# Kernel optimization log

Hardware: AMD Instinct MI355X
Metric: run time of the kernel (lower is better)

The kernel has to match this reference:

```python
import jax, jax.numpy as jnp
import numpy as np

B, CIN, COUT, K, E, H, W = 32, 128, 256, 3, 8, 64, 64


def setup_inputs() -> dict:
    key = jax.random.key(0)
    k1, k2, k3, k4 = jax.random.split(key, 4)
    x = jax.random.normal(k1, (B, CIN, H, W), dtype=jnp.float32)
    expert_weight = jax.random.normal(k2, (E, COUT, CIN, K, K), dtype=jnp.float32)
    # nn.Linear(in_channels, num_experts): weight [E, CIN], bias [E]
    bound = 1.0 / np.sqrt(CIN)
    routing_w = jax.random.uniform(k3, (E, CIN), minval=-bound, maxval=bound, dtype=jnp.float32)
    routing_b = jax.random.uniform(k4, (E,), minval=-bound, maxval=bound, dtype=jnp.float32)
    return {"x": x, "expert_weight": expert_weight, "routing_w": routing_w, "routing_b": routing_b}


def reference(x, expert_weight, routing_w, routing_b):
    # routing: global-avg-pool -> linear -> softmax over experts
    pooled = x.mean(axis=(2, 3))                             # [B, CIN]
    logits = pooled @ routing_w.T + routing_b                # [B, E]
    rweights = jax.nn.softmax(logits, axis=-1)               # [B, E]
    # per-sample combined conv weights: [B, COUT, CIN, K, K]
    cw = jnp.einsum('be,eoikl->boikl', rweights, expert_weight)

    def conv_one(xi, wi):
        # xi: [CIN, H, W], wi: [COUT, CIN, K, K]; VALID conv, stride 1
        return jax.lax.conv_general_dilated(
            xi[None], wi, window_strides=(1, 1), padding='VALID',
            dimension_numbers=('NCHW', 'OIHW', 'NCHW'))[0]

    return jax.vmap(conv_one)(x, cw)                         # [B, COUT, H-K+1, W-K+1]
```

## Files before the change

### kernel.cpp

```cpp
#include <hip/hip_runtime.h>
#include <hip/hip_bf16.h>


#define CC_B    32
#define CC_CIN  128
#define CC_COUT 256
#define CC_NP   3844
#define CC_NT   18

typedef __attribute__((ext_vector_type(8))) short bf16x8;
typedef __attribute__((ext_vector_type(4))) float f32x4;

__global__ void cc_nhwc(const float* __restrict__ x, __hip_bfloat16* __restrict__ xn,
                        float* __restrict__ psum) {
    const int b = blockIdx.x >> 6, y = blockIdx.x & 63;
    __shared__ float lds[64 * 129];
    __shared__ float sred[256];
    const int t = threadIdx.x;
    const float* src = x + (size_t)b * CC_CIN * 4096 + y * 64;
#pragma unroll
    for (int i = 0; i < 32; ++i) {
        const int idx = i * 256 + t;
        const int cin = idx >> 6, xx = idx & 63;
        lds[xx * 129 + cin] = src[(size_t)cin * 4096 + xx];
    }
    __syncthreads();
    __hip_bfloat16* dst = xn + ((size_t)b * 4096 + y * 64) * CC_CIN;
#pragma unroll
    for (int j = 0; j < 4; ++j) {
        const int cidx = j * 256 + t;
        const int xx = cidx >> 4, c8 = (cidx & 15) * 8;
        union { __hip_bfloat16 h[8]; uint4 v; } u;
#pragma unroll
        for (int jj = 0; jj < 8; ++jj) u.h[jj] = __float2bfloat16(lds[xx * 129 + c8 + jj]);
        *reinterpret_cast<uint4*>(dst + (size_t)xx * CC_CIN + c8) = u.v;
    }
    const int cin = t & 127, xh = (t >> 7) * 32;
    float s = 0.f;
#pragma unroll
    for (int xx = 0; xx < 32; ++xx) s += lds[(xh + xx) * 129 + cin];
    sred[t] = s;
    __syncthreads();
    if (t < 128) psum[((size_t)b * 64 + y) * CC_CIN + t] = sred[t] + sred[t + 128];
}

__global__ void cc_route(const float* __restrict__ psum,
                         const float* __restrict__ rw_w,
                         const float* __restrict__ rw_b,
                         float* __restrict__ rweights) {
    const int b = blockIdx.x, c = threadIdx.x;
    __shared__ float pl[128];
    __shared__ float lg[8];
    const float* p = psum + (size_t)b * 64 * CC_CIN + c;
    float s = 0.f;
#pragma unroll 8
    for (int y = 0; y < 64; ++y) s += p[(size_t)y * CC_CIN];
    pl[c] = s * (1.f / 4096.f);
    __syncthreads();
    if (c < 8) {
        const float* w = rw_w + c * CC_CIN;
        float a = rw_b[c];
#pragma unroll 8
        for (int i = 0; i < CC_CIN; ++i) a += pl[i] * w[i];
        lg[c] = a;
    }
    __syncthreads();
    if (c == 0) {
        float m = lg[0];
#pragma unroll
        for (int e = 1; e < 8; ++e) m = fmaxf(m, lg[e]);
        float ex[8], sm = 0.f;
#pragma unroll
        for (int e = 0; e < 8; ++e) { ex[e] = __expf(lg[e] - m); sm += ex[e]; }
#pragma unroll
        for (int e = 0; e < 8; ++e) rweights[b * 8 + e] = ex[e] / sm;
    }
}

__global__ void cc_combine(const float* __restrict__ ew,
                           const float* __restrict__ rw,
                           __hip_bfloat16* __restrict__ cw) {
    const int t9 = blockIdx.x >> 8;
    const int cout = blockIdx.x & 255;
    const int cin = threadIdx.x;
    __shared__ float rws[256];
    rws[cin] = rw[cin];
    rws[cin + 128] = rw[cin + 128];
    __syncthreads();
    float wv[8];
    const size_t base = ((size_t)cout * CC_CIN + cin) * 9 + t9;
#pragma unroll
    for (int e = 0; e < 8; ++e) wv[e] = ew[base + (size_t)e * (CC_COUT * CC_CIN * 9)];
#pragma unroll 4
    for (int b = 0; b < CC_B; ++b) {
        float acc = 0.f;
#pragma unroll
        for (int e = 0; e < 8; ++e) acc += rws[b * 8 + e] * wv[e];
        cw[(((size_t)b * 9 + t9) * CC_COUT + cout) * CC_CIN + cin] = __float2bfloat16(acc);
    }
}

__device__ __forceinline__ void gload_lds16(const void* g, void* l) {
    __builtin_amdgcn_global_load_lds(
        (const __attribute__((address_space(1))) unsigned int*)g,
        (__attribute__((address_space(3))) unsigned int*)l, 16, 0, 0);
}

__global__ __launch_bounds__(256, 2) void cc_conv(
    const __hip_bfloat16* __restrict__ xn,
    const __hip_bfloat16* __restrict__ cw,
    float* __restrict__ out)
{
    __shared__ __align__(16) char smem[73728];
    const int l   = blockIdx.x;
    const int xcd = l & 7, li = l >> 3;
    const int b   = 4 * xcd + li / 50;
    const int r2  = li % 50;
    const int nt  = r2 >> 1, mt = r2 & 1;
    const int m0  = mt * 128;
    const int n0  = nt * 160;

    const int tid = threadIdx.x;
    const int wid = tid >> 6, lane = tid & 63;
    const int waveM = wid >> 1, waveN = wid & 1;

    f32x4 acc[4][5];
#pragma unroll
    for (int i = 0; i < 4; ++i)
#pragma unroll
        for (int j = 0; j < 5; ++j) acc[i][j] = (f32x4){0.f, 0.f, 0.f, 0.f};

    const int gsw = (lane & 7) ^ (lane >> 3);
    int laOff[4], lbOff[5];
#pragma unroll
    for (int i = 0; i < 4; ++i) {
        const int row = wid * 32 + i * 8 + (lane >> 3);
        laOff[i] = (m0 + row) * CC_CIN + gsw * 8;
    }
#pragma unroll
    for (int i = 0; i < 5; ++i) {
        const int row = wid * 40 + i * 8 + (lane >> 3);
        int p = n0 + row; if (p > CC_NP - 1) p = CC_NP - 1;
        const int oy = p / 62, ox = p - oy * 62;
        lbOff[i] = (oy * 64 + ox) * CC_CIN + gsw * 8;
    }

    const __hip_bfloat16* cwb = cw + (size_t)b * 9 * CC_COUT * CC_CIN;
    const __hip_bfloat16* xnb = xn + (size_t)b * 4096 * CC_CIN;

    auto stageK = [&](int t) {
        const int t9 = t >> 1;
        const int ky = (t9 * 11) >> 5;
        const int kx = t9 - ky * 3;
        const int aoff = t9 * (CC_COUT * CC_CIN) + (t & 1) * 64;
        const int boff = (ky * 64 + kx) * CC_CIN + (t & 1) * 64;
        char* Ab = smem + (t & 1) * 16384 + wid * 4096;
        char* Bb = smem + 32768 + (t & 1) * 20480 + wid * 5120;
#pragma unroll
        for (int i = 0; i < 4; ++i)
            gload_lds16(cwb + aoff + laOff[i], Ab + i * 1024);
#pragma unroll
        for (int i = 0; i < 5; ++i)
            gload_lds16(xnb + boff + lbOff[i], Bb + i * 1024);
    };

    const int rl = lane & 15, q = lane >> 4;

    stageK(0);
    stageK(1);

#pragma unroll
    for (int t = 0; t < CC_NT; ++t) {
        const char* Ab = smem + (t & 1) * 16384;
        const char* Bb = smem + 32768 + (t & 1) * 20480;

        if (t < CC_NT - 1) asm volatile("s_waitcnt vmcnt(9)" ::: "memory");
        else               asm volatile("s_waitcnt vmcnt(0)" ::: "memory");
        asm volatile("s_barrier" ::: "memory");

        bf16x8 af[8], bf[10];
#pragma unroll
        for (int mf = 0; mf < 4; ++mf)
#pragma unroll
            for (int kk = 0; kk < 2; ++kk) {
                const int r = waveM * 64 + mf * 16 + rl;
                af[mf * 2 + kk] = *(const bf16x8*)(Ab + r * 128 + (((kk * 4 + q) ^ (r & 7)) * 16));
            }
#pragma unroll
        for (int nf = 0; nf < 5; ++nf)
#pragma unroll
            for (int kk = 0; kk < 2; ++kk) {
                const int r = waveN * 80 + nf * 16 + rl;
                bf[nf * 2 + kk] = *(const bf16x8*)(Bb + r * 128 + (((kk * 4 + q) ^ (r & 7)) * 16));
            }
        __builtin_amdgcn_s_setprio(1);
#pragma unroll
        for (int kk = 0; kk < 2; ++kk)
#pragma unroll
            for (int mf = 0; mf < 4; ++mf)
#pragma unroll
                for (int nf = 0; nf < 5; ++nf)
                    acc[mf][nf] = __builtin_amdgcn_mfma_f32_16x16x32_bf16(
                        af[mf * 2 + kk], bf[nf * 2 + kk], acc[mf][nf], 0, 0, 0);
        __builtin_amdgcn_s_setprio(0);

        asm volatile("s_waitcnt lgkmcnt(0)" ::: "memory");
        asm volatile("s_barrier" ::: "memory");
        if (t + 2 < CC_NT) stageK(t + 2);
    }

    const int q4 = (lane >> 4) * 4;
#pragma unroll
    for (int mf = 0; mf < 4; ++mf) {
        const int crow = m0 + waveM * 64 + mf * 16 + q4;
#pragma unroll
        for (int nf = 0; nf < 5; ++nf) {
            const int p = n0 + waveN * 80 + nf * 16 + (lane & 15);
            if (p < CC_NP) {
                const size_t ob = ((size_t)b * CC_COUT + crow) * CC_NP + p;
#pragma unroll
                for (int j = 0; j < 4; ++j) out[ob + (size_t)j * CC_NP] = acc[mf][nf][j];
            }
        }
    }
}

extern "C" void kernel_launch(void* const* d_in, const int* in_sizes, int n_in,
                              void* d_out, int out_size, void* d_ws, size_t ws_size,
                              hipStream_t stream) {
    const float* x   = (const float*)d_in[0];
    const float* ew  = (const float*)d_in[1];
    const float* rww = (const float*)d_in[2];
    const float* rwb = (const float*)d_in[3];
    float* out = (float*)d_out;
    char* ws = (char*)d_ws;

    __hip_bfloat16* xnhwc = (__hip_bfloat16*)ws;
    __hip_bfloat16* cwcmb = (__hip_bfloat16*)(ws + 33554432);
    float* psum   = (float*)(ws + 52428800);
    float* rwts   = (float*)(ws + 53493760);

    cc_nhwc<<<dim3(CC_B * 64), dim3(256), 0, stream>>>(x, xnhwc, psum);
    cc_route<<<dim3(CC_B), dim3(128), 0, stream>>>(psum, rww, rwb, rwts);
    cc_combine<<<dim3(9 * CC_COUT), dim3(128), 0, stream>>>(ew, rwts, cwcmb);
    cc_conv<<<dim3(1600), dim3(256), 0, stream>>>(xnhwc, cwcmb, out);
}
```

Before: 124.4 us.

## Load conv input fragments directly to registers, keep only weights in LDS

The B operand (input pixels) is no longer staged through LDS. Each lane now loads its bf16x8 fragments straight from global memory into a double-buffered register array, one step ahead of use. The weight tile still goes through LDS, but the pipeline is restructured so the next A stage is issued right after the barrier, and LDS shrinks from 72KB to 32KB. This removes LDS write/read traffic and one barrier per step, and may allow more resident blocks. The cost is many more VGPRs for the double-buffered B fragments, uncoalesced 16-byte global loads with overlap across kernel taps, and vmcnt counts that must match the exact order in which loads are issued.

```diff
diff --git a/kernel.cpp b/kernel.cpp
--- a/kernel.cpp
+++ b/kernel.cpp
@@ -111,7 +111,7 @@
     const __hip_bfloat16* __restrict__ cw,
     float* __restrict__ out)
 {
-    __shared__ __align__(16) char smem[73728];
+    __shared__ __align__(16) char smem[32768];
     const int l   = blockIdx.x;
     const int xcd = l & 7, li = l >> 3;
     const int b   = 4 * xcd + li / 50;
@@ -131,54 +131,63 @@
         for (int j = 0; j < 5; ++j) acc[i][j] = (f32x4){0.f, 0.f, 0.f, 0.f};
 
     const int gsw = (lane & 7) ^ (lane >> 3);
-    int laOff[4], lbOff[5];
+    int laOff[4];
 #pragma unroll
     for (int i = 0; i < 4; ++i) {
         const int row = wid * 32 + i * 8 + (lane >> 3);
         laOff[i] = (m0 + row) * CC_CIN + gsw * 8;
     }
-#pragma unroll
-    for (int i = 0; i < 5; ++i) {
-        const int row = wid * 40 + i * 8 + (lane >> 3);
-        int p = n0 + row; if (p > CC_NP - 1) p = CC_NP - 1;
-        const int oy = p / 62, ox = p - oy * 62;
-        lbOff[i] = (oy * 64 + ox) * CC_CIN + gsw * 8;
-    }
 
     const __hip_bfloat16* cwb = cw + (size_t)b * 9 * CC_COUT * CC_CIN;
     const __hip_bfloat16* xnb = xn + (size_t)b * 4096 * CC_CIN;
 
-    auto stageK = [&](int t) {
+    auto stageA = [&](int t) {
+        const int t9 = t >> 1;
+        const int aoff = t9 * (CC_COUT * CC_CIN) + (t & 1) * 64;
+        char* Ab = smem + (t & 1) * 16384 + wid * 4096;
+#pragma unroll
+        for (int i = 0; i < 4; ++i)
+            gload_lds16(cwb + aoff + laOff[i], Ab + i * 1024);
+    };
+
+    const int rl = lane & 15, q = lane >> 4;
+
+    int pixq[5];
+#pragma unroll
+    for (int nf = 0; nf < 5; ++nf) {
+        int p = n0 + waveN * 80 + nf * 16 + rl;
+        if (p > CC_NP - 1) p = CC_NP - 1;
+        const int oy = p / 62, ox = p - oy * 62;
+        pixq[nf] = (oy * 64 + ox) * CC_CIN + q * 8;
+    }
+
+    bf16x8 bfr[2][10];
+    auto loadB = [&](int t) {
         const int t9 = t >> 1;
         const int ky = (t9 * 11) >> 5;
         const int kx = t9 - ky * 3;
-        const int aoff = t9 * (CC_COUT * CC_CIN) + (t & 1) * 64;
-        const int boff = (ky * 64 + kx) * CC_CIN + (t & 1) * 64;
-        char* Ab = smem + (t & 1) * 16384 + wid * 4096;
-        char* Bb = smem + 32768 + (t & 1) * 20480 + wid * 5120;
-#pragma unroll
-        for (int i = 0; i < 4; ++i)
-            gload_lds16(cwb + aoff + laOff[i], Ab + i * 1024);
-#pragma unroll
-        for (int i = 0; i < 5; ++i)
-            gload_lds16(xnb + boff + lbOff[i], Bb + i * 1024);
+        const int kd = (ky * 64 + kx) * CC_CIN + (t & 1) * 64;
+#pragma unroll
+        for (int nf = 0; nf < 5; ++nf)
+#pragma unroll
+            for (int kk = 0; kk < 2; ++kk)
+                bfr[t & 1][nf * 2 + kk] =
+                    *(const bf16x8*)(xnb + pixq[nf] + kd + kk * 32);
     };
 
-    const int rl = lane & 15, q = lane >> 4;
-
-    stageK(0);
-    stageK(1);
+    stageA(0);
+    loadB(0);
 
 #pragma unroll
     for (int t = 0; t < CC_NT; ++t) {
         const char* Ab = smem + (t & 1) * 16384;
-        const char* Bb = smem + 32768 + (t & 1) * 20480;
-
-        if (t < CC_NT - 1) asm volatile("s_waitcnt vmcnt(9)" ::: "memory");
-        else               asm volatile("s_waitcnt vmcnt(0)" ::: "memory");
+
+        asm volatile("s_waitcnt vmcnt(10)" ::: "memory");
         asm volatile("s_barrier" ::: "memory");
 
-        bf16x8 af[8], bf[10];
+        if (t + 1 < CC_NT) stageA(t + 1);
+
+        bf16x8 af[8];
 #pragma unroll
         for (int mf = 0; mf < 4; ++mf)
 #pragma unroll
@@ -186,13 +195,13 @@
                 const int r = waveM * 64 + mf * 16 + rl;
                 af[mf * 2 + kk] = *(const bf16x8*)(Ab + r * 128 + (((kk * 4 + q) ^ (r & 7)) * 16));
             }
-#pragma unroll
-        for (int nf = 0; nf < 5; ++nf)
-#pragma unroll
-            for (int kk = 0; kk < 2; ++kk) {
-                const int r = waveN * 80 + nf * 16 + rl;
-                bf[nf * 2 + kk] = *(const bf16x8*)(Bb + r * 128 + (((kk * 4 + q) ^ (r & 7)) * 16));
-            }
+
+        if (t + 1 < CC_NT) loadB(t + 1);
+
+        if (t < CC_NT - 1) asm volatile("s_waitcnt vmcnt(14)" ::: "memory");
+        else               asm volatile("s_waitcnt vmcnt(0)" ::: "memory");
+        asm volatile("s_waitcnt lgkmcnt(0)" ::: "memory");
+
         __builtin_amdgcn_s_setprio(1);
 #pragma unroll
         for (int kk = 0; kk < 2; ++kk)
@@ -201,12 +210,8 @@
 #pragma unroll
                 for (int nf = 0; nf < 5; ++nf)
                     acc[mf][nf] = __builtin_amdgcn_mfma_f32_16x16x32_bf16(
-                        af[mf * 2 + kk], bf[nf * 2 + kk], acc[mf][nf], 0, 0, 0);
+                        af[mf * 2 + kk], bfr[t & 1][nf * 2 + kk], acc[mf][nf], 0, 0, 0);
         __builtin_amdgcn_s_setprio(0);
-
-        asm volatile("s_waitcnt lgkmcnt(0)" ::: "memory");
-        asm volatile("s_barrier" ::: "memory");
-        if (t + 2 < CC_NT) stageK(t + 2);
     }
 
     const int q4 = (lane >> 4) * 4;
```

Result: slower. 191.1 us (+53.6%).
